# Optimization experiments

Hardware: AMD Instinct MI355X
Metric: run time of the kernel (lower is better)

## Reference

```python
import jax, jax.numpy as jnp
import numpy as np

SCALE = (4, 4)
PORTION = 0.5


def setup_inputs() -> dict:
    key = jax.random.key(0)
    x = jax.random.normal(key, (16, 512, 64, 64), dtype=jnp.float32)
    return {"x": x}


def _shift_scale(x, s0, s1):
    # x: (b, shift, h, w); cyclic shuffle of the S=s0*s1 channel groups,
    # with a spatially-varying shift amount over the (s0, s1) sub-grid.
    b, c, h, w = x.shape
    S = s0 * s1
    cps = c // S
    # (b, S, cps, s0, h/s0, s1, w/s1)
    y = x.reshape(b, S, cps, s0, h // s0, s1, w // s1)
    # -> (b, S, cps, h/s0, w/s1, s0, s1) -> (b, S, cps, h/s0, w/s1, S)
    y = y.transpose(0, 1, 2, 4, 6, 3, 5).reshape(b, S, cps, h // s0, w // s1, S)
    # index[s, k] = (s + k) mod S  (cyclic gather along last axis)
    idx = (jnp.arange(S)[:, None] + jnp.arange(S)[None, :]) % S
    y = jnp.take_along_axis(y, idx.reshape(1, S, 1, 1, 1, S), axis=5)
    # undo the spatial regrouping: (b, c, h/s0, w/s1, s0, s1) -> (b, c, h, w)
    y = y.reshape(b, c, h // s0, w // s1, s0, s1)
    y = y.transpose(0, 1, 4, 2, 5, 3).reshape(b, c, h, w)
    return y


def reference(x):
    s0, s1 = SCALE
    S = s0 * s1
    b, c, h, w = x.shape
    shift = int(PORTION * c)
    shift = (shift // S) * S  # floor to multiple of S (matches torch code)
    keep_x = x[:, : c - shift]
    shift_x = _shift_scale(x[:, c - shift :], s0, s1)
    return jnp.concatenate([keep_x, shift_x], axis=1)
```

## Files before the change

### kernel.cpp

```cpp
#include <hip/hip_runtime.h>


#define B 16
#define C 512
#define H 64
#define W 64
#define W4 (W / 4)

__global__ __launch_bounds__(256) void GlobalShift2dV2Portion_kernel(
    const float4* __restrict__ in, float4* __restrict__ out) {
    int i = blockIdx.x * 256 + threadIdx.x;
    int w4 = i & 15;
    int t  = i >> 4;
    int h  = t & 63;
    int bc = t >> 6;
    int ch = bc & 511;
    if (ch < 256) {
        out[i] = in[i];
    } else {
        int s     = (ch - 256) >> 4;
        int t_in  = (s + ((h >> 4) << 2) + (w4 >> 2)) & 15;
        int h_in  = ((t_in >> 2) << 4) | (h & 15);
        int w4_in = ((t_in & 3) << 2) | (w4 & 3);
        int j     = ((bc << 6) + h_in) * W4 + w4_in;
        out[i] = in[j];
    }
}

extern "C" void kernel_launch(void* const* d_in, const int* in_sizes, int n_in,
                              void* d_out, int out_size, void* d_ws, size_t ws_size,
                              hipStream_t stream) {
    const float4* in = (const float4*)d_in[0];
    float4* out = (float4*)d_out;
    int total4 = in_sizes[0] / 4;
    int blocks = total4 / 256;
    GlobalShift2dV2Portion_kernel<<<blocks, 256, 0, stream>>>(in, out);
}
```

Measured before the change: 222.5 us.

## Stage each channel image in LDS and use nontemporal stores

Each block now handles one full 64x64 channel image. It loads the image with coalesced reads into shared memory, then writes the shuffled output from LDS. Keep-channels are copied directly. All stores are nontemporal to avoid polluting cache. This swaps the scattered global gather for an LDS gather, at the cost of one barrier and 16KB of LDS per block, which may reduce occupancy.

```diff
diff --git a/kernel.cpp b/kernel.cpp
--- a/kernel.cpp
+++ b/kernel.cpp
@@ -1,38 +1,53 @@
 #include <hip/hip_runtime.h>
 
 
-#define B 16
-#define C 512
-#define H 64
-#define W 64
-#define W4 (W / 4)
+#define CC   512
+#define IMG4 1024
+
+typedef float f32x4 __attribute__((ext_vector_type(4)));
 
 __global__ __launch_bounds__(256) void GlobalShift2dV2Portion_kernel(
-    const float4* __restrict__ in, float4* __restrict__ out) {
-    int i = blockIdx.x * 256 + threadIdx.x;
-    int w4 = i & 15;
-    int t  = i >> 4;
-    int h  = t & 63;
-    int bc = t >> 6;
-    int ch = bc & 511;
-    if (ch < 256) {
-        out[i] = in[i];
-    } else {
-        int s     = (ch - 256) >> 4;
-        int t_in  = (s + ((h >> 4) << 2) + (w4 >> 2)) & 15;
-        int h_in  = ((t_in >> 2) << 4) | (h & 15);
-        int w4_in = ((t_in & 3) << 2) | (w4 & 3);
-        int j     = ((bc << 6) + h_in) * W4 + w4_in;
-        out[i] = in[j];
+    const f32x4* __restrict__ in, f32x4* __restrict__ out) {
+  __shared__ f32x4 lds[IMG4];
+  const int bc   = blockIdx.x;
+  const int ch   = bc & (CC - 1);
+  const int base = bc << 10;
+  const int tid  = threadIdx.x;
+
+  if (ch < CC / 2) {
+#pragma unroll
+    for (int k = 0; k < 4; ++k) {
+      const int o = (k << 8) + tid;
+      __builtin_nontemporal_store(in[base + o], &out[base + o]);
     }
+    return;
+  }
+
+#pragma unroll
+  for (int k = 0; k < 4; ++k) {
+    const int o = (k << 8) + tid;
+    lds[o] = in[base + o];
+  }
+  __syncthreads();
+
+  const int s = (ch - CC / 2) >> 4;
+#pragma unroll
+  for (int k = 0; k < 4; ++k) {
+    const int o     = (k << 8) + tid;
+    const int w4    = o & 15;
+    const int h     = o >> 4;
+    const int t_in  = (s + ((h >> 4) << 2) + (w4 >> 2)) & 15;
+    const int h_in  = ((t_in >> 2) << 4) | (h & 15);
+    const int w4_in = ((t_in & 3) << 2) | (w4 & 3);
+    __builtin_nontemporal_store(lds[(h_in << 4) | w4_in], &out[base + o]);
+  }
 }
 
 extern "C" void kernel_launch(void* const* d_in, const int* in_sizes, int n_in,
                               void* d_out, int out_size, void* d_ws, size_t ws_size,
                               hipStream_t stream) {
-    const float4* in = (const float4*)d_in[0];
-    float4* out = (float4*)d_out;
-    int total4 = in_sizes[0] / 4;
-    int blocks = total4 / 256;
-    GlobalShift2dV2Portion_kernel<<<blocks, 256, 0, stream>>>(in, out);
+  const f32x4* in = (const f32x4*)d_in[0];
+  f32x4* out = (f32x4*)d_out;
+  const int blocks = in_sizes[0] / (IMG4 * 4);
+  GlobalShift2dV2Portion_kernel<<<blocks, 256, 0, stream>>>(in, out);
 }
```

Measured after the change: 227.5 us. 1.02x slower.
